# Kernel tuning notes

Measured on AMD Instinct MI355X. Metric: run time of the kernel, lower is better.

The kernel has to match this reference:

```python
import jax, jax.numpy as jnp
import numpy as np

NUM_GENES = 9229
NUM_FEATURES = 3
BATCH = 4096


def setup_inputs() -> dict:
    key = jax.random.key(0)
    k1, k2, k3 = jax.random.split(key, 3)
    x = jax.random.normal(k1, (BATCH, NUM_GENES * NUM_FEATURES), dtype=jnp.float32)
    weights = jax.random.normal(k2, (NUM_GENES * NUM_FEATURES,), dtype=jnp.float32)
    bias = 0.1 * jax.random.normal(k3, (NUM_GENES,), dtype=jnp.float32)
    return {"x": x, "weights": weights, "bias": bias}


def reference(x, weights, bias):
    # Block-diagonal scatter + mm is equivalent to a per-gene weighted sum
    # over the feature dimension:
    # x: [B, G*F] -> [B, G, F]; weights: [G*F] -> [G, F]
    B = x.shape[0]
    xg = x.reshape(B, NUM_GENES, NUM_FEATURES)
    wg = weights.reshape(NUM_GENES, NUM_FEATURES)
    out = jnp.einsum("bgf,gf->bg", xg, wg) + bias  # [B, G]
    return out
```

## Files before the change

kernel.cpp:

```cpp
#include <hip/hip_runtime.h>


#define G        9229u
#define GFW      27687u
#define NUNIT    147664u
#define NWAVES   8192u
#define WEXT_N   (27687 + 768)
#define BEXT_OFF 28456
#define BEXT_N   (9229 + 256)
#define WS_FLOATS (BEXT_OFF + BEXT_N)

typedef float f32x4 __attribute__((ext_vector_type(4)));

__global__ __launch_bounds__(256) void build_ext_kernel(
    const float* __restrict__ w, const float* __restrict__ bias,
    float* __restrict__ ws) {
    const int i = (int)blockIdx.x * 256 + (int)threadIdx.x;
    if (i < WEXT_N) {
        ws[i] = w[i >= (int)GFW ? i - (int)GFW : i];
    } else {
        const int k = i - WEXT_N;
        if (k < BEXT_N) ws[BEXT_OFF + k] = bias[k >= (int)G ? k - (int)G : k];
    }
}

__global__ __launch_bounds__(256, 8) void diag_class_kernel(
    const float* __restrict__ x,
    const float* __restrict__ ws,
    float* __restrict__ out) {

    const float* wext = ws;
    const float* bext = ws + BEXT_OFF;

    const int t  = (int)(threadIdx.x & 63);
    const int wv = (int)blockIdx.x * 4 + (int)(threadIdx.x >> 6);

    const int tm    = t % 3;
    const bool last = (t == 63);
    const int srcA = (3 * t) & 63;
    const int srcC = (3 * t + 1) & 63;
    const int srcD = (3 * t + 2) & 63;

    const unsigned cnt  = 18u + ((unsigned)wv < 208u ? 1u : 0u);
    unsigned idx        = 18u * (unsigned)wv + ((unsigned)wv < 208u ? (unsigned)wv : 208u);
    const unsigned end  = idx + cnt;

    while (idx < end) {
        const unsigned c    = idx >> 4;
        const unsigned k0   = idx & 15u;
        const unsigned rem  = end - (c << 4);
        const unsigned kend = rem < 16u ? rem : 16u;
        const unsigned g0   = (256u * c) % G;
        const unsigned wf0  = 3u * g0;

        const float4 w0 = *reinterpret_cast<const float4*>(wext + wf0 + 4 * t);
        const float4 w1 = *reinterpret_cast<const float4*>(wext + wf0 + 256 + 4 * t);
        const float4 w2 = *reinterpret_cast<const float4*>(wext + wf0 + 512 + 4 * t);
        const float4 bv = *reinterpret_cast<const float4*>(bext + g0 + 4 * t);

        for (unsigned k = k0; k < kend; ++k) {
            const unsigned u  = c + G * k;
            const float* xr   = x + 768u * u;

            const f32x4 v0 = __builtin_nontemporal_load(
                reinterpret_cast<const f32x4*>(xr + 4 * t));
            const f32x4 v1 = __builtin_nontemporal_load(
                reinterpret_cast<const f32x4*>(xr + 256 + 4 * t));
            const f32x4 v2 = __builtin_nontemporal_load(
                reinterpret_cast<const f32x4*>(xr + 512 + 4 * t));

            const float a0 = v0.x * w0.x, a1 = v0.y * w0.y, a2 = v0.z * w0.z, a3 = v0.w * w0.w;
            const float q01_0 = a0 + a1, q23_0 = a2 + a3;
            const float q012_0 = q01_0 + a2, q123_0 = q23_0 + a1;
            const float b0 = v1.x * w1.x, b1 = v1.y * w1.y, b2 = v1.z * w1.z, b3 = v1.w * w1.w;
            const float q01_1 = b0 + b1, q23_1 = b2 + b3;
            const float q012_1 = q01_1 + b2, q123_1 = q23_1 + b1;
            const float c0 = v2.x * w2.x, c1 = v2.y * w2.y, c2 = v2.z * w2.z, c3 = v2.w * w2.w;
            const float q01_2 = c0 + c1, q23_2 = c2 + c3;
            const float q012_2 = q01_2 + c2, q123_2 = q23_2 + c1;

            const float s0 = (tm == 1) ? q01_0 : a0;
            const float s1 = (tm == 0) ? q01_1 : b0;
            const float s2 = (tm == 2) ? q01_2 : c0;
            const float r0 = __shfl(s0, (t + 1) & 63);
            const float r1 = __shfl(s1, (t + 1) & 63);
            const float r2 = __shfl(s2, (t + 1) & 63);
            const float E0 = last ? r1 : r0;
            const float E1 = last ? r2 : r1;
            const float E2 = r2;

            const float bb0 = a3 + E0, bb1 = b3 + E1, bb2 = c3 + E2;
            const float cc0 = q23_0 + E0, cc1 = q23_1 + E1, cc2 = q23_2 + E2;

            const float A  = (tm == 0) ? q012_0 : (tm == 2) ? q012_1 : q012_2;
            const float Bv = (tm == 0) ? bb0   : (tm == 2) ? bb1   : bb2;
            const float C  = (tm == 1) ? cc0   : (tm == 0) ? cc1   : cc2;
            const float D  = (tm == 2) ? q123_0 : (tm == 1) ? q123_1 : q123_2;

            f32x4 o;
            o.x = __shfl(A,  srcA) + bv.x;
            o.y = __shfl(Bv, srcA) + bv.y;
            o.z = __shfl(C,  srcC) + bv.z;
            o.w = __shfl(D,  srcD) + bv.w;

            __builtin_nontemporal_store(
                o, reinterpret_cast<f32x4*>(out + 256u * u + 4 * t));
        }
        idx = (c << 4) + kend;
    }
}

extern "C" void kernel_launch(void* const* d_in, const int* in_sizes, int n_in,
                              void* d_out, int out_size, void* d_ws, size_t ws_size,
                              hipStream_t stream) {
    const float* x    = (const float*)d_in[0];
    const float* w    = (const float*)d_in[1];
    const float* bias = (const float*)d_in[2];
    float* out        = (float*)d_out;
    float* ws         = (float*)d_ws;

    build_ext_kernel<<<(WEXT_N + BEXT_N + 255) / 256, 256, 0, stream>>>(w, bias, ws);
    diag_class_kernel<<<2048, 256, 0, stream>>>(x, ws, out);
}
```

Before: 122.0 us.

## Replace weight-class contiguous work split with flat grid-stride unit loop

Drops the scheme that grouped units sharing one weight/bias slice (stride G apart) so each wave reused loaded weights across up to 16 units. Instead each wave walks units with a grid stride of NWAVES and reloads weights and bias for every unit, which touches x and out in a more sequential order across the device. The output store also changes from nontemporal to a normal store. The trade is more weight/bias loads, which should mostly hit cache, in exchange for more contiguous DRAM streaming and simpler control flow.

```diff
diff --git a/kernel.cpp b/kernel.cpp
--- a/kernel.cpp
+++ b/kernel.cpp
@@ -1,13 +1,13 @@
 #include <hip/hip_runtime.h>
 
 
-#define G        9229u
-#define GFW      27687u
-#define NUNIT    147664u
-#define NWAVES   8192u
-#define WEXT_N   (27687 + 768)
+#define G       9229
+#define GFW     27687
+#define NUNIT   147664
+#define NWAVES  8192
+#define WEXT_N  (GFW + 768)
 #define BEXT_OFF 28456
-#define BEXT_N   (9229 + 256)
+#define BEXT_N  (G + 256)
 #define WS_FLOATS (BEXT_OFF + BEXT_N)
 
 typedef float f32x4 __attribute__((ext_vector_type(4)));
@@ -17,14 +17,14 @@
     float* __restrict__ ws) {
     const int i = (int)blockIdx.x * 256 + (int)threadIdx.x;
     if (i < WEXT_N) {
-        ws[i] = w[i >= (int)GFW ? i - (int)GFW : i];
+        ws[i] = w[i >= GFW ? i - GFW : i];
     } else {
         const int k = i - WEXT_N;
-        if (k < BEXT_N) ws[BEXT_OFF + k] = bias[k >= (int)G ? k - (int)G : k];
+        if (k < BEXT_N) ws[BEXT_OFF + k] = bias[k >= G ? k - G : k];
     }
 }
 
-__global__ __launch_bounds__(256, 8) void diag_class_kernel(
+__global__ __launch_bounds__(256, 8) void diag_flat_kernel(
     const float* __restrict__ x,
     const float* __restrict__ ws,
     float* __restrict__ out) {
@@ -41,72 +41,59 @@
     const int srcC = (3 * t + 1) & 63;
     const int srcD = (3 * t + 2) & 63;
 
-    const unsigned cnt  = 18u + ((unsigned)wv < 208u ? 1u : 0u);
-    unsigned idx        = 18u * (unsigned)wv + ((unsigned)wv < 208u ? (unsigned)wv : 208u);
-    const unsigned end  = idx + cnt;
+    for (unsigned u = (unsigned)wv; u < NUNIT; u += NWAVES) {
+        const unsigned O0  = 256u * u;
+        const unsigned g0  = O0 % (unsigned)G;
+        const unsigned wf0 = 3u * g0;
+        const float* xr = x + 768u * u;
 
-    while (idx < end) {
-        const unsigned c    = idx >> 4;
-        const unsigned k0   = idx & 15u;
-        const unsigned rem  = end - (c << 4);
-        const unsigned kend = rem < 16u ? rem : 16u;
-        const unsigned g0   = (256u * c) % G;
-        const unsigned wf0  = 3u * g0;
+        const f32x4 v0 = __builtin_nontemporal_load(
+            reinterpret_cast<const f32x4*>(xr + 4 * t));
+        const f32x4 v1 = __builtin_nontemporal_load(
+            reinterpret_cast<const f32x4*>(xr + 256 + 4 * t));
+        const f32x4 v2 = __builtin_nontemporal_load(
+            reinterpret_cast<const f32x4*>(xr + 512 + 4 * t));
 
         const float4 w0 = *reinterpret_cast<const float4*>(wext + wf0 + 4 * t);
         const float4 w1 = *reinterpret_cast<const float4*>(wext + wf0 + 256 + 4 * t);
         const float4 w2 = *reinterpret_cast<const float4*>(wext + wf0 + 512 + 4 * t);
         const float4 bv = *reinterpret_cast<const float4*>(bext + g0 + 4 * t);
 
-        for (unsigned k = k0; k < kend; ++k) {
-            const unsigned u  = c + G * k;
-            const float* xr   = x + 768u * u;
+        const float a0 = v0.x * w0.x, a1 = v0.y * w0.y, a2 = v0.z * w0.z, a3 = v0.w * w0.w;
+        const float q01_0 = a0 + a1, q23_0 = a2 + a3;
+        const float q012_0 = q01_0 + a2, q123_0 = q23_0 + a1;
+        const float b0 = v1.x * w1.x, b1 = v1.y * w1.y, b2 = v1.z * w1.z, b3 = v1.w * w1.w;
+        const float q01_1 = b0 + b1, q23_1 = b2 + b3;
+        const float q012_1 = q01_1 + b2, q123_1 = q23_1 + b1;
+        const float c0 = v2.x * w2.x, c1 = v2.y * w2.y, c2 = v2.z * w2.z, c3 = v2.w * w2.w;
+        const float q01_2 = c0 + c1, q23_2 = c2 + c3;
+        const float q012_2 = q01_2 + c2, q123_2 = q23_2 + c1;
 
-            const f32x4 v0 = __builtin_nontemporal_load(
-                reinterpret_cast<const f32x4*>(xr + 4 * t));
-            const f32x4 v1 = __builtin_nontemporal_load(
-                reinterpret_cast<const f32x4*>(xr + 256 + 4 * t));
-            const f32x4 v2 = __builtin_nontemporal_load(
-                reinterpret_cast<const f32x4*>(xr + 512 + 4 * t));
+        const float s0 = (tm == 1) ? q01_0 : a0;
+        const float s1 = (tm == 0) ? q01_1 : b0;
+        const float s2 = (tm == 2) ? q01_2 : c0;
+        const float r0 = __shfl(s0, (t + 1) & 63);
+        const float r1 = __shfl(s1, (t + 1) & 63);
+        const float r2 = __shfl(s2, (t + 1) & 63);
+        const float E0 = last ? r1 : r0;
+        const float E1 = last ? r2 : r1;
+        const float E2 = r2;
 
-            const float a0 = v0.x * w0.x, a1 = v0.y * w0.y, a2 = v0.z * w0.z, a3 = v0.w * w0.w;
-            const float q01_0 = a0 + a1, q23_0 = a2 + a3;
-            const float q012_0 = q01_0 + a2, q123_0 = q23_0 + a1;
-            const float b0 = v1.x * w1.x, b1 = v1.y * w1.y, b2 = v1.z * w1.z, b3 = v1.w * w1.w;
-            const float q01_1 = b0 + b1, q23_1 = b2 + b3;
-            const float q012_1 = q01_1 + b2, q123_1 = q23_1 + b1;
-            const float c0 = v2.x * w2.x, c1 = v2.y * w2.y, c2 = v2.z * w2.z, c3 = v2.w * w2.w;
-            const float q01_2 = c0 + c1, q23_2 = c2 + c3;
-            const float q012_2 = q01_2 + c2, q123_2 = q23_2 + c1;
+        const float bb0 = a3 + E0, bb1 = b3 + E1, bb2 = c3 + E2;
+        const float cc0 = q23_0 + E0, cc1 = q23_1 + E1, cc2 = q23_2 + E2;
 
-            const float s0 = (tm == 1) ? q01_0 : a0;
-            const float s1 = (tm == 0) ? q01_1 : b0;
-            const float s2 = (tm == 2) ? q01_2 : c0;
-            const float r0 = __shfl(s0, (t + 1) & 63);
-            const float r1 = __shfl(s1, (t + 1) & 63);
-            const float r2 = __shfl(s2, (t + 1) & 63);
-            const float E0 = last ? r1 : r0;
-            const float E1 = last ? r2 : r1;
-            const float E2 = r2;
+        const float A  = (tm == 0) ? q012_0 : (tm == 2) ? q012_1 : q012_2;
+        const float Bv = (tm == 0) ? bb0   : (tm == 2) ? bb1   : bb2;
+        const float C  = (tm == 1) ? cc0   : (tm == 0) ? cc1   : cc2;
+        const float D  = (tm == 2) ? q123_0 : (tm == 1) ? q123_1 : q123_2;
 
-            const float bb0 = a3 + E0, bb1 = b3 + E1, bb2 = c3 + E2;
-            const float cc0 = q23_0 + E0, cc1 = q23_1 + E1, cc2 = q23_2 + E2;
+        f32x4 o;
+        o.x = __shfl(A,  srcA) + bv.x;
+        o.y = __shfl(Bv, srcA) + bv.y;
+        o.z = __shfl(C,  srcC) + bv.z;
+        o.w = __shfl(D,  srcD) + bv.w;
 
-            const float A  = (tm == 0) ? q012_0 : (tm == 2) ? q012_1 : q012_2;
-            const float Bv = (tm == 0) ? bb0   : (tm == 2) ? bb1   : bb2;
-            const float C  = (tm == 1) ? cc0   : (tm == 0) ? cc1   : cc2;
-            const float D  = (tm == 2) ? q123_0 : (tm == 1) ? q123_1 : q123_2;
-
-            f32x4 o;
-            o.x = __shfl(A,  srcA) + bv.x;
-            o.y = __shfl(Bv, srcA) + bv.y;
-            o.z = __shfl(C,  srcC) + bv.z;
-            o.w = __shfl(D,  srcD) + bv.w;
-
-            __builtin_nontemporal_store(
-                o, reinterpret_cast<f32x4*>(out + 256u * u + 4 * t));
-        }
-        idx = (c << 4) + kend;
+        *reinterpret_cast<f32x4*>(out + O0 + 4 * t) = o;
     }
 }
 
@@ -120,5 +107,5 @@
     float* ws         = (float*)d_ws;
 
     build_ext_kernel<<<(WEXT_N + BEXT_N + 255) / 256, 256, 0, stream>>>(w, bias, ws);
-    diag_class_kernel<<<2048, 256, 0, stream>>>(x, ws, out);
+    diag_flat_kernel<<<2048, 256, 0, stream>>>(x, ws, out);
 }
```

Measured after the change: 122.0 us. Within noise of the previous version (-0.0%).
